# Kernel tuning notes

Hardware: AMD Instinct MI355X
Metric: run time of the kernel (lower is better)

## Reference

```python
import jax, jax.numpy as jnp
import numpy as np

TOP_K = 2
NUM_EXPERTS = 8
EPS = 1e-9


def setup_inputs() -> dict:
    key = jax.random.key(0)
    ks = jax.random.split(key, 6)
    B, S, H, E, F = 2, 1024, 1024, NUM_EXPERTS, 512
    hidden_states = jax.random.normal(ks[0], (B, S, H), dtype=jnp.float32)
    gate_w = jax.random.normal(ks[1], (E, H), dtype=jnp.float32) * 0.02
    gate_up_proj = jax.random.normal(ks[2], (E, H, 2 * F), dtype=jnp.float32) * 0.02
    down_proj = jax.random.normal(ks[3], (E, F, H), dtype=jnp.float32) * 0.02
    # modality in {-1, 0, 1}: -1 text, 1 vision, 0 special/unassigned
    token_modality = (jax.random.randint(ks[4], (B * S,), 0, 3) - 1).astype(jnp.int32)
    expert_modality = (jax.random.randint(ks[5], (E,), 0, 3) - 1).astype(jnp.int32)
    return {
        "hidden_states": hidden_states,
        "gate_w": gate_w,
        "gate_up_proj": gate_up_proj,
        "down_proj": down_proj,
        "token_modality": token_modality,
        "expert_modality": expert_modality,
    }


def reference(hidden_states, gate_w, gate_up_proj, down_proj, token_modality, expert_modality):
    B, S, H = hidden_states.shape
    bs = B * S
    E, K = NUM_EXPERTS, TOP_K
    x = hidden_states.reshape(bs, H)

    # ---- router: GEMM + softmax + top-k + renorm ----
    router_logits = x @ gate_w.T                              # [bs, E]
    probs = jax.nn.softmax(router_logits, axis=-1)
    rw, sel = jax.lax.top_k(probs, K)                         # [bs, K]
    rw = rw / jnp.sum(rw, axis=-1, keepdims=True)

    # ---- modality-masked expert skip (prefill branch: seq_length > 1) ----
    tok_mod_slots = jnp.broadcast_to(token_modality[:, None], (bs, K))  # [bs, K]
    exp_mod_slots = expert_modality[sel]                                # [bs, K]
    valid = (tok_mod_slots != 0) & (exp_mod_slots != 0)
    mismatch = valid & ((tok_mod_slots * exp_mod_slots) == -1)

    sel_flat = sel.reshape(-1)
    valid_count = jax.ops.segment_sum(valid.reshape(-1).astype(jnp.int32), sel_flat, num_segments=E)
    mismatch_count = jax.ops.segment_sum(mismatch.reshape(-1).astype(jnp.int32), sel_flat, num_segments=E)
    skip_expert = (valid_count > 0) & (mismatch_count == valid_count) & (expert_modality != 0)

    zero_mask = skip_expert[sel]                              # [bs, K]
    rw = jnp.where(zero_mask, 0.0, rw)
    sum_w2 = jnp.sum(rw, axis=-1, keepdims=True)
    rw = jnp.where(sum_w2 > 0, rw / jnp.maximum(sum_w2, EPS), rw)

    # ---- scatter top-k weights into dense [bs, E] routing matrix ----
    dense_w = jnp.zeros((bs, E), dtype=rw.dtype).at[jnp.arange(bs)[:, None], sel].set(rw)

    # ---- fused experts: SiLU-gated MLP per expert, combined by routing weights ----
    gu = jnp.einsum("th,ehf->tef", x, gate_up_proj)           # [bs, E, 2F]
    g, u = jnp.split(gu, 2, axis=-1)
    act = jax.nn.silu(g) * u                                  # [bs, E, F]
    out = jnp.einsum("tef,efh,te->th", act, down_proj, dense_w)
    return out.reshape(B, S, H)
```

## Files before the change

kernel.cpp:

```cpp
#include <hip/hip_runtime.h>
#include <math.h>

#define BS 2048
#define H  1024
#define E  8
#define F  512

typedef __attribute__((ext_vector_type(8))) short bf16x8;
typedef __attribute__((ext_vector_type(4))) float f32x4;
typedef unsigned short u16;
typedef unsigned int u32;

__device__ inline u16 f2bf(float f) {
    u32 u = __float_as_uint(f);
    return (u16)((u + 0x7fffu + ((u >> 16) & 1u)) >> 16);
}

__device__ __forceinline__ void async_cp16(const u16* g, u16* l) {
    __builtin_amdgcn_global_load_lds(
        (const __attribute__((address_space(1))) void*)g,
        (__attribute__((address_space(3))) void*)l, 16, 0, 0);
}


__global__ __launch_bounds__(256) void prep_weights_kernel(
    const float* __restrict__ g, const float* __restrict__ d,
    u16* __restrict__ gt, u16* __restrict__ dt, int* __restrict__ counters)
{
    int b = blockIdx.x;
    int tid = threadIdx.x;
    if (b == 0 && tid < 24) counters[tid] = 0;

    const float* src; u16* dst_base; int e, kt, nt, K, Nn;
    if (b < 2048) {
        e = b >> 8; int rem = b & 255; kt = rem >> 4; nt = rem & 15;
        src = g + (size_t)e * 1048576; dst_base = gt + (size_t)e * 1048576; K = 1024; Nn = 1024;
    } else {
        int b2 = b - 2048; e = b2 >> 7; int rem = b2 & 127; kt = rem >> 4; nt = rem & 15;
        src = d + (size_t)e * 524288; dst_base = dt + (size_t)e * 524288; K = 512; Nn = 1024;
    }
    int k0 = kt * 64, n0 = nt * 64;
    __shared__ float t[64][68];
    int r = tid >> 2, c4 = tid & 3;
    const float* srow = src + (size_t)(k0 + r) * Nn + n0 + c4 * 16;
#pragma unroll
    for (int i = 0; i < 4; i++) {
        float4 v = *(const float4*)(srow + i * 4);
        *(float4*)&t[r][c4 * 16 + i * 4] = v;
    }
    __syncthreads();
    u16 o[16];
#pragma unroll
    for (int m = 0; m < 16; m++) o[m] = f2bf(t[c4 * 16 + m][r]);
    u16* dst = dst_base + (size_t)(n0 + r) * K + k0 + c4 * 16;
    uint4 q0, q1;
    q0.x = (u32)o[0] | ((u32)o[1] << 16);  q0.y = (u32)o[2] | ((u32)o[3] << 16);
    q0.z = (u32)o[4] | ((u32)o[5] << 16);  q0.w = (u32)o[6] | ((u32)o[7] << 16);
    q1.x = (u32)o[8] | ((u32)o[9] << 16);  q1.y = (u32)o[10] | ((u32)o[11] << 16);
    q1.z = (u32)o[12] | ((u32)o[13] << 16); q1.w = (u32)o[14] | ((u32)o[15] << 16);
    *(uint4*)dst = q0;
    *(uint4*)(dst + 8) = q1;
}

__global__ __launch_bounds__(256) void router_kernel(
    const float* __restrict__ x, const float* __restrict__ gate_w,
    const int* __restrict__ tok_mod, const int* __restrict__ exp_mod,
    int* __restrict__ counters, int2* __restrict__ sel_out, float2* __restrict__ w_out,
    u16* __restrict__ xb, float* __restrict__ out)
{
    int tid = threadIdx.x;
    int wv = tid >> 6, lane = tid & 63;
    int token = blockIdx.x * 4 + wv;
    float4 z = make_float4(0.f, 0.f, 0.f, 0.f);
    float4* orow4 = (float4*)(out + (size_t)token * H);
#pragma unroll
    for (int i = 0; i < 4; i++) orow4[lane + 64 * i] = z;

    const float4* xr4 = (const float4*)(x + (size_t)token * H);
    const float4* gw4 = (const float4*)gate_w;
    float acc[E];
#pragma unroll
    for (int e = 0; e < E; e++) acc[e] = 0.f;
#pragma unroll
    for (int i = 0; i < 4; i++) {
        int idx = lane + 64 * i;
        float4 xv = xr4[idx];
        ushort4 pk;
        pk.x = f2bf(xv.x); pk.y = f2bf(xv.y); pk.z = f2bf(xv.z); pk.w = f2bf(xv.w);
        *(ushort4*)(xb + (size_t)token * H + idx * 4) = pk;
#pragma unroll
        for (int e = 0; e < E; e++) {
            float4 g = gw4[e * 256 + idx];
            acc[e] += xv.x * g.x + xv.y * g.y + xv.z * g.z + xv.w * g.w;
        }
    }
#pragma unroll
    for (int e = 0; e < E; e++) {
#pragma unroll
        for (int off = 32; off > 0; off >>= 1) acc[e] += __shfl_down(acc[e], off, 64);
    }
    if (lane == 0) {
        float m = acc[0];
#pragma unroll
        for (int e = 1; e < E; e++) m = fmaxf(m, acc[e]);
        float p[E]; float s = 0.f;
#pragma unroll
        for (int e = 0; e < E; e++) { p[e] = expf(acc[e] - m); s += p[e]; }
        float inv = 1.f / s;
#pragma unroll
        for (int e = 0; e < E; e++) p[e] *= inv;
        int i0 = 0; float p0 = p[0];
#pragma unroll
        for (int e = 1; e < E; e++) if (p[e] > p0) { p0 = p[e]; i0 = e; }
        int i1 = -1; float p1 = -1.f;
#pragma unroll
        for (int e = 0; e < E; e++) if (e != i0 && p[e] > p1) { p1 = p[e]; i1 = e; }
        float rs = 1.f / (p0 + p1);
        float w0 = p0 * rs, w1 = p1 * rs;
        int tm = tok_mod[token];
        int em0 = exp_mod[i0], em1 = exp_mod[i1];
        bool v0 = (tm != 0) && (em0 != 0);
        bool v1 = (tm != 0) && (em1 != 0);
        bool mm0 = v0 && (tm * em0 == -1);
        bool mm1 = v1 && (tm * em1 == -1);
        if (v0)  atomicAdd(&counters[i0], 1);
        if (v1)  atomicAdd(&counters[i1], 1);
        if (mm0) atomicAdd(&counters[8 + i0], 1);
        if (mm1) atomicAdd(&counters[8 + i1], 1);
        sel_out[token] = make_int2(i0, i1);
        w_out[token] = make_float2(w0, w1);
    }
}

__global__ __launch_bounds__(256) void finalize_kernel(
    const int* __restrict__ exp_mod, int* __restrict__ counters,
    const int2* __restrict__ sel_in, const float2* __restrict__ w_in,
    int* __restrict__ tok_list, float* __restrict__ w_list)
{
    int t = blockIdx.x * 256 + threadIdx.x;
    if (t >= BS) return;
    bool skip[E];
#pragma unroll
    for (int e = 0; e < E; e++) {
        int vc = counters[e], mc = counters[8 + e];
        skip[e] = (vc > 0) && (mc == vc) && (exp_mod[e] != 0);
    }
    int2 sel = sel_in[t];
    float2 w = w_in[t];
    float w0 = skip[sel.x] ? 0.f : w.x;
    float w1 = skip[sel.y] ? 0.f : w.y;
    float s = w0 + w1;
    if (s > 0.f) { float inv = 1.f / fmaxf(s, 1e-9f); w0 *= inv; w1 *= inv; }
    if (w0 > 0.f) {
        int pos = atomicAdd(&counters[16 + sel.x], 1);
        tok_list[sel.x * BS + pos] = t; w_list[sel.x * BS + pos] = w0;
    }
    if (w1 > 0.f) {
        int pos = atomicAdd(&counters[16 + sel.y], 1);
        tok_list[sel.y * BS + pos] = t; w_list[sel.y * BS + pos] = w1;
    }
}

__global__ __launch_bounds__(256) void gu_mfma_kernel(
    const u16* __restrict__ xb, const u16* __restrict__ gup_t,
    const int* __restrict__ counters, const int* __restrict__ tok_list,
    const float* __restrict__ w_list, u16* __restrict__ act)
{
    int e = blockIdx.z;
    int n = counters[16 + e];
    int t0 = blockIdx.y * 64;
    if (t0 >= n) return;
    int f0 = blockIdx.x * 64;
    int base = 0;
#pragma unroll
    for (int i = 0; i < E; i++) if (i < e) base += counters[16 + i];

    __shared__ __align__(16) u16 Asl[2][64 * 64];
    __shared__ __align__(16) u16 Bsl[2][128 * 64];

    int tid = threadIdx.x;
    int wv = tid >> 6, lane = tid & 63;
    int l16 = lane & 15, quad = lane >> 4;
    int wm = wv & 1, wn = wv >> 1;

    int lr = lane >> 3, lc = lane & 7;
    int r0 = wv * 8 + lr, r1 = r0 + 32;
    int tokA0 = tok_list[e * BS + min(t0 + r0, n - 1)];
    int tokA1 = tok_list[e * BS + min(t0 + r1, n - 1)];
    const u16* agp0 = xb + (size_t)tokA0 * H + (size_t)((lc ^ (r0 & 7)) * 8);
    const u16* agp1 = xb + (size_t)tokA1 * H + (size_t)((lc ^ (r1 & 7)) * 8);
    int alo0 = r0 * 64 + lc * 8, alo1 = r1 * 64 + lc * 8;
    const u16* gb = gup_t + ((size_t)e << 20);
    const u16* bgp[4]; int blo[4];
#pragma unroll
    for (int j = 0; j < 4; j++) {
        int c = j * 32 + wv * 8 + lr;
        int gcol = (c < 64) ? (f0 + c) : (512 + f0 + (c - 64));
        bgp[j] = gb + (size_t)gcol * H + (size_t)((lc ^ (c & 7)) * 8);
        blo[j] = c * 64 + lc * 8;
    }

    f32x4 acc[2][4];
#pragma unroll
    for (int i = 0; i < 2; i++)
#pragma unroll
        for (int j = 0; j < 4; j++) acc[i][j] = (f32x4){0.f, 0.f, 0.f, 0.f};

    async_cp16(agp0, &Asl[0][alo0]);
    async_cp16(agp1, &Asl[0][alo1]);
#pragma unroll
    for (int j = 0; j < 4; j++) async_cp16(bgp[j], &Bsl[0][blo[j]]);

    int sw = l16 & 7;
    int p = 0;
    for (int k0 = 0; k0 < H; k0 += 64) {
        __syncthreads();
        if (k0 + 64 < H) {
            int q = p ^ 1;
            async_cp16(agp0 + k0 + 64, &Asl[q][alo0]);
            async_cp16(agp1 + k0 + 64, &Asl[q][alo1]);
#pragma unroll
            for (int j = 0; j < 4; j++) async_cp16(bgp[j] + k0 + 64, &Bsl[q][blo[j]]);
        }
#pragma unroll
        for (int s = 0; s < 2; s++) {
            int ch = ((s * 4 + quad) ^ sw) * 8;
            bf16x8 af[2], bfr[4];
#pragma unroll
            for (int i = 0; i < 2; i++)
                af[i] = *(const bf16x8*)&Asl[p][(wm * 32 + i * 16 + l16) * 64 + ch];
#pragma unroll
            for (int j = 0; j < 4; j++) {
                int col = (j < 2) ? (wn * 32 + j * 16 + l16) : (64 + wn * 32 + (j - 2) * 16 + l16);
                bfr[j] = *(const bf16x8*)&Bsl[p][col * 64 + ch];
            }
#pragma unroll
            for (int i = 0; i < 2; i++)
#pragma unroll
                for (int j = 0; j < 4; j++)
                    acc[i][j] = __builtin_amdgcn_mfma_f32_16x16x32_bf16(af[i], bfr[j], acc[i][j], 0, 0, 0);
        }
        p ^= 1;
    }
#pragma unroll
    for (int i = 0; i < 2; i++)
#pragma unroll
        for (int r = 0; r < 4; r++) {
            int R = t0 + wm * 32 + i * 16 + quad * 4 + r;
            if (R < n) {
                float w = w_list[e * BS + R];
                size_t rowoff = (size_t)(base + R) * F + f0 + wn * 32 + l16;
#pragma unroll
                for (int j = 0; j < 2; j++) {
                    float g = acc[i][j][r], u = acc[i][j + 2][r];
                    float v = (g / (1.f + expf(-g))) * u * w;
                    act[rowoff + j * 16] = f2bf(v);
                }
            }
        }
}

__global__ __launch_bounds__(256) void down_mfma_kernel(
    const u16* __restrict__ act, const u16* __restrict__ down_t,
    const int* __restrict__ counters, const int* __restrict__ tok_list,
    float* __restrict__ out)
{
    int e = blockIdx.z;
    int n = counters[16 + e];
    int t0 = blockIdx.y * 64;
    if (t0 >= n) return;
    int h0 = blockIdx.x * 128;
    int base = 0;
#pragma unroll
    for (int i = 0; i < E; i++) if (i < e) base += counters[16 + i];

    __shared__ __align__(16) u16 Asl[2][64 * 64];
    __shared__ __align__(16) u16 Bsl[2][128 * 64];

    int tid = threadIdx.x;
    int wv = tid >> 6, lane = tid & 63;
    int l16 = lane & 15, quad = lane >> 4;
    int wm = wv & 1, wn = wv >> 1;

    int lr = lane >> 3, lc = lane & 7;
    int r0 = wv * 8 + lr, r1 = r0 + 32;
    const u16* agp0 = act + (size_t)(base + min(t0 + r0, n - 1)) * F + (size_t)((lc ^ (r0 & 7)) * 8);
    const u16* agp1 = act + (size_t)(base + min(t0 + r1, n - 1)) * F + (size_t)((lc ^ (r1 & 7)) * 8);
    int alo0 = r0 * 64 + lc * 8, alo1 = r1 * 64 + lc * 8;
    const u16* db = down_t + ((size_t)e << 19);
    const u16* bgp[4]; int blo[4];
#pragma unroll
    for (int j = 0; j < 4; j++) {
        int c = j * 32 + wv * 8 + lr;
        bgp[j] = db + (size_t)(h0 + c) * F + (size_t)((lc ^ (c & 7)) * 8);
        blo[j] = c * 64 + lc * 8;
    }

    f32x4 acc[2][4];
#pragma unroll
    for (int i = 0; i < 2; i++)
#pragma unroll
        for (int j = 0; j < 4; j++) acc[i][j] = (f32x4){0.f, 0.f, 0.f, 0.f};

    async_cp16(agp0, &Asl[0][alo0]);
    async_cp16(agp1, &Asl[0][alo1]);
#pragma unroll
    for (int j = 0; j < 4; j++) async_cp16(bgp[j], &Bsl[0][blo[j]]);

    int sw = l16 & 7;
    int p = 0;
    for (int k0 = 0; k0 < F; k0 += 64) {
        __syncthreads();
        if (k0 + 64 < F) {
            int q = p ^ 1;
            async_cp16(agp0 + k0 + 64, &Asl[q][alo0]);
            async_cp16(agp1 + k0 + 64, &Asl[q][alo1]);
#pragma unroll
            for (int j = 0; j < 4; j++) async_cp16(bgp[j] + k0 + 64, &Bsl[q][blo[j]]);
        }
#pragma unroll
        for (int s = 0; s < 2; s++) {
            int ch = ((s * 4 + quad) ^ sw) * 8;
            bf16x8 af[2], bfr[4];
#pragma unroll
            for (int i = 0; i < 2; i++)
                af[i] = *(const bf16x8*)&Asl[p][(wm * 32 + i * 16 + l16) * 64 + ch];
#pragma unroll
            for (int j = 0; j < 4; j++)
                bfr[j] = *(const bf16x8*)&Bsl[p][(wn * 64 + j * 16 + l16) * 64 + ch];
#pragma unroll
            for (int i = 0; i < 2; i++)
#pragma unroll
                for (int j = 0; j < 4; j++)
                    acc[i][j] = __builtin_amdgcn_mfma_f32_16x16x32_bf16(af[i], bfr[j], acc[i][j], 0, 0, 0);
        }
        p ^= 1;
    }
#pragma unroll
    for (int i = 0; i < 2; i++)
#pragma unroll
        for (int r = 0; r < 4; r++) {
            int R = t0 + wm * 32 + i * 16 + quad * 4 + r;
            if (R < n) {
                int tok = tok_list[e * BS + R];
                float* orow = out + (size_t)tok * H + h0 + wn * 64 + l16;
#pragma unroll
                for (int j = 0; j < 4; j++)
                    atomicAdd(&orow[j * 16], acc[i][j][r]);
            }
        }
}

extern "C" void kernel_launch(void* const* d_in, const int* in_sizes, int n_in,
                              void* d_out, int out_size, void* d_ws, size_t ws_size,
                              hipStream_t stream)
{
    const float* x       = (const float*)d_in[0];
    const float* gate_w  = (const float*)d_in[1];
    const float* gup     = (const float*)d_in[2];
    const float* down    = (const float*)d_in[3];
    const int*   tok_mod = (const int*)d_in[4];
    const int*   exp_mod = (const int*)d_in[5];
    float* out = (float*)d_out;

    char* ws = (char*)d_ws;
    int*    counters = (int*)ws;
    int2*   sel      = (int2*)(ws + 4096);
    float2* wsel     = (float2*)(ws + 20480);
    int*    tok_list = (int*)(ws + 36864);
    float*  w_list   = (float*)(ws + 102400);
    u16*    x_bf     = (u16*)(ws + 167936);
    u16*    gup_t    = (u16*)(ws + 4362240);
    u16*    down_t   = (u16*)(ws + 21139456);
    u16*    act      = (u16*)(ws + 29528064);

    prep_weights_kernel<<<3072, 256, 0, stream>>>(gup, down, gup_t, down_t, counters);
    router_kernel<<<BS / 4, 256, 0, stream>>>(x, gate_w, tok_mod, exp_mod, counters, sel, wsel, x_bf, out);
    finalize_kernel<<<BS / 256, 256, 0, stream>>>(exp_mod, counters, sel, wsel, tok_list, w_list);
    gu_mfma_kernel<<<dim3(8, 32, E), 256, 0, stream>>>(x_bf, gup_t, counters, tok_list, w_list, act);
    down_mfma_kernel<<<dim3(8, 32, E), 256, 0, stream>>>(act, down_t, counters, tok_list, out);
}
```

Measured before the change: 185.8 us.

## Fuse weight prep with router and move routing counts into single-block finalize

Merges the weight transpose/convert kernel and the router kernel into one launch, with block index selecting the role, so both run concurrently and one launch is removed. The router no longer does global atomics; it packs valid/mismatch flags into the selection indices. Finalize becomes a single 1024-thread block that counts with shared-memory atomics and builds the per-expert token lists, then writes the counts to global memory. Using one block serializes finalize on a single CU, and token-list order within each expert may change.

```diff
diff --git a/kernel.cpp b/kernel.cpp
--- a/kernel.cpp
+++ b/kernel.cpp
@@ -23,54 +23,52 @@
 }
 
 
-__global__ __launch_bounds__(256) void prep_weights_kernel(
-    const float* __restrict__ g, const float* __restrict__ d,
-    u16* __restrict__ gt, u16* __restrict__ dt, int* __restrict__ counters)
+__global__ __launch_bounds__(256) void prep_router_kernel(
+    const float* __restrict__ gup, const float* __restrict__ dwn,
+    u16* __restrict__ gt, u16* __restrict__ dt,
+    const float* __restrict__ x, const float* __restrict__ gate_w,
+    const int* __restrict__ tok_mod, const int* __restrict__ exp_mod,
+    int2* __restrict__ sel_out, float2* __restrict__ w_out,
+    u16* __restrict__ xb, float* __restrict__ out)
 {
     int b = blockIdx.x;
     int tid = threadIdx.x;
-    if (b == 0 && tid < 24) counters[tid] = 0;
-
-    const float* src; u16* dst_base; int e, kt, nt, K, Nn;
-    if (b < 2048) {
-        e = b >> 8; int rem = b & 255; kt = rem >> 4; nt = rem & 15;
-        src = g + (size_t)e * 1048576; dst_base = gt + (size_t)e * 1048576; K = 1024; Nn = 1024;
-    } else {
-        int b2 = b - 2048; e = b2 >> 7; int rem = b2 & 127; kt = rem >> 4; nt = rem & 15;
-        src = d + (size_t)e * 524288; dst_base = dt + (size_t)e * 524288; K = 512; Nn = 1024;
-    }
-    int k0 = kt * 64, n0 = nt * 64;
-    __shared__ float t[64][68];
-    int r = tid >> 2, c4 = tid & 3;
-    const float* srow = src + (size_t)(k0 + r) * Nn + n0 + c4 * 16;
-#pragma unroll
-    for (int i = 0; i < 4; i++) {
-        float4 v = *(const float4*)(srow + i * 4);
-        *(float4*)&t[r][c4 * 16 + i * 4] = v;
-    }
-    __syncthreads();
-    u16 o[16];
-#pragma unroll
-    for (int m = 0; m < 16; m++) o[m] = f2bf(t[c4 * 16 + m][r]);
-    u16* dst = dst_base + (size_t)(n0 + r) * K + k0 + c4 * 16;
-    uint4 q0, q1;
-    q0.x = (u32)o[0] | ((u32)o[1] << 16);  q0.y = (u32)o[2] | ((u32)o[3] << 16);
-    q0.z = (u32)o[4] | ((u32)o[5] << 16);  q0.w = (u32)o[6] | ((u32)o[7] << 16);
-    q1.x = (u32)o[8] | ((u32)o[9] << 16);  q1.y = (u32)o[10] | ((u32)o[11] << 16);
-    q1.z = (u32)o[12] | ((u32)o[13] << 16); q1.w = (u32)o[14] | ((u32)o[15] << 16);
-    *(uint4*)dst = q0;
-    *(uint4*)(dst + 8) = q1;
-}
-
-__global__ __launch_bounds__(256) void router_kernel(
-    const float* __restrict__ x, const float* __restrict__ gate_w,
-    const int* __restrict__ tok_mod, const int* __restrict__ exp_mod,
-    int* __restrict__ counters, int2* __restrict__ sel_out, float2* __restrict__ w_out,
-    u16* __restrict__ xb, float* __restrict__ out)
-{
-    int tid = threadIdx.x;
+
+    if (b < 3072) {
+        const float* src; u16* dst_base; int e, kt, nt, K, Nn;
+        if (b < 2048) {
+            e = b >> 8; int rem = b & 255; kt = rem >> 4; nt = rem & 15;
+            src = gup + (size_t)e * 1048576; dst_base = gt + (size_t)e * 1048576; K = 1024; Nn = 1024;
+        } else {
+            int b2 = b - 2048; e = b2 >> 7; int rem = b2 & 127; kt = rem >> 4; nt = rem & 15;
+            src = dwn + (size_t)e * 524288; dst_base = dt + (size_t)e * 524288; K = 512; Nn = 1024;
+        }
+        int k0 = kt * 64, n0 = nt * 64;
+        __shared__ float t[64][68];
+        int r = tid >> 2, c4 = tid & 3;
+        const float* srow = src + (size_t)(k0 + r) * Nn + n0 + c4 * 16;
+#pragma unroll
+        for (int i = 0; i < 4; i++) {
+            float4 v = *(const float4*)(srow + i * 4);
+            *(float4*)&t[r][c4 * 16 + i * 4] = v;
+        }
+        __syncthreads();
+        u16 o[16];
+#pragma unroll
+        for (int m = 0; m < 16; m++) o[m] = f2bf(t[c4 * 16 + m][r]);
+        u16* dst = dst_base + (size_t)(n0 + r) * K + k0 + c4 * 16;
+        uint4 q0, q1;
+        q0.x = (u32)o[0] | ((u32)o[1] << 16);  q0.y = (u32)o[2] | ((u32)o[3] << 16);
+        q0.z = (u32)o[4] | ((u32)o[5] << 16);  q0.w = (u32)o[6] | ((u32)o[7] << 16);
+        q1.x = (u32)o[8] | ((u32)o[9] << 16);  q1.y = (u32)o[10] | ((u32)o[11] << 16);
+        q1.z = (u32)o[12] | ((u32)o[13] << 16); q1.w = (u32)o[14] | ((u32)o[15] << 16);
+        *(uint4*)dst = q0;
+        *(uint4*)(dst + 8) = q1;
+        return;
+    }
+
     int wv = tid >> 6, lane = tid & 63;
-    int token = blockIdx.x * 4 + wv;
+    int token = (b - 3072) * 4 + wv;
     float4 z = make_float4(0.f, 0.f, 0.f, 0.f);
     float4* orow4 = (float4*)(out + (size_t)token * H);
 #pragma unroll
@@ -119,46 +117,61 @@
         float w0 = p0 * rs, w1 = p1 * rs;
         int tm = tok_mod[token];
         int em0 = exp_mod[i0], em1 = exp_mod[i1];
-        bool v0 = (tm != 0) && (em0 != 0);
-        bool v1 = (tm != 0) && (em1 != 0);
-        bool mm0 = v0 && (tm * em0 == -1);
-        bool mm1 = v1 && (tm * em1 == -1);
-        if (v0)  atomicAdd(&counters[i0], 1);
-        if (v1)  atomicAdd(&counters[i1], 1);
-        if (mm0) atomicAdd(&counters[8 + i0], 1);
-        if (mm1) atomicAdd(&counters[8 + i1], 1);
-        sel_out[token] = make_int2(i0, i1);
+        int v0 = (tm != 0) && (em0 != 0);
+        int v1 = (tm != 0) && (em1 != 0);
+        int mm0 = v0 && (tm * em0 == -1);
+        int mm1 = v1 && (tm * em1 == -1);
+        sel_out[token] = make_int2(i0 | (v0 << 8) | (mm0 << 9),
+                                   i1 | (v1 << 8) | (mm1 << 9));
         w_out[token] = make_float2(w0, w1);
     }
 }
 
-__global__ __launch_bounds__(256) void finalize_kernel(
+__global__ __launch_bounds__(1024) void finalize_kernel(
     const int* __restrict__ exp_mod, int* __restrict__ counters,
     const int2* __restrict__ sel_in, const float2* __restrict__ w_in,
     int* __restrict__ tok_list, float* __restrict__ w_list)
 {
-    int t = blockIdx.x * 256 + threadIdx.x;
-    if (t >= BS) return;
+    __shared__ int vcnt[E], mcnt[E], gpos[E];
+    int tid = threadIdx.x;
+    if (tid < E) { vcnt[tid] = 0; mcnt[tid] = 0; gpos[tid] = 0; }
+    __syncthreads();
+#pragma unroll
+    for (int h = 0; h < 2; h++) {
+        int t = tid + h * 1024;
+        int2 s = sel_in[t];
+        int i0 = s.x & 7, i1 = s.y & 7;
+        if (s.x & 256) atomicAdd(&vcnt[i0], 1);
+        if (s.x & 512) atomicAdd(&mcnt[i0], 1);
+        if (s.y & 256) atomicAdd(&vcnt[i1], 1);
+        if (s.y & 512) atomicAdd(&mcnt[i1], 1);
+    }
+    __syncthreads();
     bool skip[E];
 #pragma unroll
-    for (int e = 0; e < E; e++) {
-        int vc = counters[e], mc = counters[8 + e];
-        skip[e] = (vc > 0) && (mc == vc) && (exp_mod[e] != 0);
-    }
-    int2 sel = sel_in[t];
-    float2 w = w_in[t];
-    float w0 = skip[sel.x] ? 0.f : w.x;
-    float w1 = skip[sel.y] ? 0.f : w.y;
-    float s = w0 + w1;
-    if (s > 0.f) { float inv = 1.f / fmaxf(s, 1e-9f); w0 *= inv; w1 *= inv; }
-    if (w0 > 0.f) {
-        int pos = atomicAdd(&counters[16 + sel.x], 1);
-        tok_list[sel.x * BS + pos] = t; w_list[sel.x * BS + pos] = w0;
-    }
-    if (w1 > 0.f) {
-        int pos = atomicAdd(&counters[16 + sel.y], 1);
-        tok_list[sel.y * BS + pos] = t; w_list[sel.y * BS + pos] = w1;
-    }
+    for (int e = 0; e < E; e++)
+        skip[e] = (vcnt[e] > 0) && (mcnt[e] == vcnt[e]) && (exp_mod[e] != 0);
+#pragma unroll
+    for (int h = 0; h < 2; h++) {
+        int t = tid + h * 1024;
+        int2 s = sel_in[t];
+        int i0 = s.x & 7, i1 = s.y & 7;
+        float2 w = w_in[t];
+        float w0 = skip[i0] ? 0.f : w.x;
+        float w1 = skip[i1] ? 0.f : w.y;
+        float sm = w0 + w1;
+        if (sm > 0.f) { float inv = 1.f / fmaxf(sm, 1e-9f); w0 *= inv; w1 *= inv; }
+        if (w0 > 0.f) {
+            int pos = atomicAdd(&gpos[i0], 1);
+            tok_list[i0 * BS + pos] = t; w_list[i0 * BS + pos] = w0;
+        }
+        if (w1 > 0.f) {
+            int pos = atomicAdd(&gpos[i1], 1);
+            tok_list[i1 * BS + pos] = t; w_list[i1 * BS + pos] = w1;
+        }
+    }
+    __syncthreads();
+    if (tid < E) counters[16 + tid] = gpos[tid];
 }
 
 __global__ __launch_bounds__(256) void gu_mfma_kernel(
@@ -374,9 +387,10 @@
     u16*    down_t   = (u16*)(ws + 21139456);
     u16*    act      = (u16*)(ws + 29528064);
 
-    prep_weights_kernel<<<3072, 256, 0, stream>>>(gup, down, gup_t, down_t, counters);
-    router_kernel<<<BS / 4, 256, 0, stream>>>(x, gate_w, tok_mod, exp_mod, counters, sel, wsel, x_bf, out);
-    finalize_kernel<<<BS / 256, 256, 0, stream>>>(exp_mod, counters, sel, wsel, tok_list, w_list);
+    prep_router_kernel<<<3584, 256, 0, stream>>>(gup, down, gup_t, down_t,
+                                                 x, gate_w, tok_mod, exp_mod,
+                                                 sel, wsel, x_bf, out);
+    finalize_kernel<<<1, 1024, 0, stream>>>(exp_mod, counters, sel, wsel, tok_list, w_list);
     gu_mfma_kernel<<<dim3(8, 32, E), 256, 0, stream>>>(x_bf, gup_t, counters, tok_list, w_list, act);
     down_mfma_kernel<<<dim3(8, 32, E), 256, 0, stream>>>(act, down_t, counters, tok_list, out);
 }
```

New measurement: 157.3 us. -15.4%, faster.
